# Kernel optimization log

Measured on AMD Instinct MI355X. Metric: run time of the kernel, lower is better.

## Reference

```python
import jax, jax.numpy as jnp
import numpy as np

N = 50000      # nodes
E = 600000     # edges
D_IN = 5
D_H = 128
EPS = 1e-5     # BatchNorm1d default eps


def batch_norm(x, gamma, beta):
    # training-mode BN over the node dimension (biased variance)
    m = jnp.mean(x, axis=0)
    v = jnp.var(x, axis=0)
    return (x - m) * jax.lax.rsqrt(v + EPS) * gamma + beta


def gcn_conv(x, W, b, src, dst, w):
    # PyG GCNConv: linear transform, add self-loops (weight 1),
    # symmetric normalization D^-1/2 A D^-1/2, scatter-add to dst, + bias.
    x = x @ W                                   # [N, out]
    n = x.shape[0]
    loop = jnp.arange(n)
    src = jnp.concatenate([src, loop])
    dst = jnp.concatenate([dst, loop])
    w = jnp.concatenate([w, jnp.ones((n,), w.dtype)])
    deg = jax.ops.segment_sum(w, dst, num_segments=n)
    dis = jnp.where(deg > 0, jax.lax.rsqrt(jnp.maximum(deg, 1e-12)), 0.0)
    norm = dis[src] * w * dis[dst]              # [E+N]
    msgs = norm[:, None] * x[src]               # gather + scale
    return jax.ops.segment_sum(msgs, dst, num_segments=n) + b


def setup_inputs() -> dict:
    key = jax.random.key(0)
    ks = jax.random.split(key, 20)
    s_in = 1.0 / np.sqrt(D_IN)
    s_h = 1.0 / np.sqrt(D_H)
    return {
        "h": jax.random.normal(ks[0], (N, D_IN), jnp.float32),
        "edge_index": jax.random.randint(ks[1], (2, E), 0, N),
        "edge_weight": jax.random.uniform(ks[2], (E,), jnp.float32),
        "g0": 1.0 + 0.1 * jax.random.normal(ks[3], (D_IN,), jnp.float32),
        "be0": 0.1 * jax.random.normal(ks[4], (D_IN,), jnp.float32),
        "W1": jax.random.normal(ks[5], (D_IN, D_H), jnp.float32) * s_in,
        "b1": jax.random.normal(ks[6], (D_H,), jnp.float32) * s_in,
        "g1": 1.0 + 0.1 * jax.random.normal(ks[7], (D_H,), jnp.float32),
        "be1": 0.1 * jax.random.normal(ks[8], (D_H,), jnp.float32),
        "W2": jax.random.normal(ks[9], (D_H, D_H), jnp.float32) * s_h,
        "b2": jax.random.normal(ks[10], (D_H,), jnp.float32) * s_h,
        "g2": 1.0 + 0.1 * jax.random.normal(ks[11], (D_H,), jnp.float32),
        "be2": 0.1 * jax.random.normal(ks[12], (D_H,), jnp.float32),
        "Wmu": jax.random.normal(ks[13], (D_H, D_H), jnp.float32) * s_h,
        "bmu": jax.random.normal(ks[14], (D_H,), jnp.float32) * s_h,
        "Wls": jax.random.normal(ks[15], (D_H, D_H), jnp.float32) * s_h,
        "bls": jax.random.normal(ks[16], (D_H,), jnp.float32) * s_h,
    }


def reference(h, edge_index, edge_weight, g0, be0, W1, b1, g1, be1,
              W2, b2, g2, be2, Wmu, bmu, Wls, bls):
    src, dst = edge_index[0], edge_index[1]
    h = batch_norm(h, g0, be0)
    h = jax.nn.relu(batch_norm(gcn_conv(h, W1, b1, src, dst, edge_weight), g1, be1))
    # dropout p=0.1 treated as eval-mode (identity)
    h = jax.nn.relu(batch_norm(gcn_conv(h, W2, b2, src, dst, edge_weight), g2, be2))
    mu = h @ Wmu + bmu
    log_std = h @ Wls + bls
    return (mu, log_std)
```

## Files before the change

### kernel.cpp

```cpp
#include <hip/hip_runtime.h>

#define N_NODES 50000
#define N_EDGES 600000
#define D_IN 5
#define D_H 128
#define BN_EPS 1e-5f
#define SCAN_BLOCKS ((N_NODES + 255) / 256)
#define DEG_BLOCKS ((N_EDGES + 255) / 256)
#define FIX_SCALE 16777216.0f
#define FIX_INV   (1.0f / 16777216.0f)

typedef __bf16 bf16x8 __attribute__((ext_vector_type(8)));
typedef float  f32x4  __attribute__((ext_vector_type(4)));

__device__ inline unsigned short f2bfb(float f) {
    unsigned u = __builtin_bit_cast(unsigned, f);
    unsigned r = u + 0x7fffu + ((u >> 16) & 1u);
    return (unsigned short)(r >> 16);
}
__device__ inline float bflo(unsigned u) { return __builtin_bit_cast(float, u << 16); }
__device__ inline float bfhi(unsigned u) { return __builtin_bit_cast(float, u & 0xffff0000u); }

__device__ inline void stage_b(const unsigned short* __restrict__ Bt,
                               uint4* __restrict__ lds, int t)
{
#pragma unroll
    for (int i = 0; i < 8; ++i) {
        int slot = i * 256 + t;
        int fid = slot >> 6;
        int l = slot & 63;
        int row = (fid >> 2) * 16 + (l & 15);
        int boff = ((l >> 4) * 16 + (fid & 3) * 64) >> 1;
        lds[slot] = *(const uint4*)(Bt + row * D_H + boff);
    }
}

__global__ __launch_bounds__(256) void k_prep(const float* __restrict__ W2,
                                              const float* __restrict__ Wmu,
                                              const float* __restrict__ Wls,
                                              unsigned short* __restrict__ T2,
                                              unsigned short* __restrict__ Tmu,
                                              unsigned short* __restrict__ Tls,
                                              const float* __restrict__ h,
                                              float* __restrict__ stats0,
                                              const int* __restrict__ dst,
                                              const float* __restrict__ w,
                                              unsigned long long* __restrict__ degcnt,
                                              int* __restrict__ rank)
{
    __shared__ float ss[D_IN], sq[D_IN];
    int b = blockIdx.x;
    int t = threadIdx.x;
    if (b < 192) {
        int mat = b >> 6;
        int idx = (b & 63) * 256 + t;
        const float* W = (mat == 0) ? W2 : (mat == 1) ? Wmu : Wls;
        unsigned short* T = (mat == 0) ? T2 : (mat == 1) ? Tmu : Tls;
        int k = idx >> 7, n = idx & 127;
        T[n * D_H + k] = f2bfb(W[idx]);
    } else if (b < 192 + SCAN_BLOCKS) {
        if (t < D_IN) { ss[t] = 0.f; sq[t] = 0.f; }
        __syncthreads();
        int node = (b - 192) * 256 + t;
        float v[D_IN];
#pragma unroll
        for (int f = 0; f < D_IN; ++f)
            v[f] = (node < N_NODES) ? h[node * D_IN + f] : 0.f;
        int lane = t & 63;
#pragma unroll
        for (int f = 0; f < D_IN; ++f) {
            float s = v[f], q = v[f] * v[f];
            for (int off = 32; off > 0; off >>= 1) {
                s += __shfl_down(s, off);
                q += __shfl_down(q, off);
            }
            if (lane == 0) { atomicAdd(&ss[f], s); atomicAdd(&sq[f], q); }
        }
        __syncthreads();
        if (t < D_IN) {
            atomicAdd(&stats0[t], ss[t]);
            atomicAdd(&stats0[D_IN + t], sq[t]);
        }
    } else {
        int e = (b - 192 - SCAN_BLOCKS) * 256 + t;
        if (e < N_EDGES) {
            int d = dst[e];
            unsigned long long fx = (unsigned long long)(w[e] * FIX_SCALE + 0.5f);
            unsigned long long old = atomicAdd(degcnt + d, (1ull << 40) | fx);
            rank[e] = (int)(old >> 40);
        }
    }
}

__global__ __launch_bounds__(256) void k_scan1(const unsigned long long* __restrict__ degcnt,
                                               float* __restrict__ dis,
                                               int* __restrict__ blocksums)
{
    __shared__ int sm[256];
    int t = threadIdx.x;
    int i = blockIdx.x * 256 + t;
    int c = 0;
    if (i < N_NODES) {
        unsigned long long v = degcnt[i];
        c = (int)(v >> 40);
        float deg = (float)(v & ((1ull << 40) - 1)) * FIX_INV;
        dis[i] = rsqrtf(deg + 1.0f);
    }
    sm[t] = c;
    __syncthreads();
    for (int off = 128; off > 0; off >>= 1) {
        if (t < off) sm[t] += sm[t + off];
        __syncthreads();
    }
    if (t == 0) blocksums[blockIdx.x] = sm[0];
}

__global__ __launch_bounds__(256) void k_scan2(int* __restrict__ blocksums,
                                               int* __restrict__ rowptr)
{
    __shared__ int sm[256];
    int t = threadIdx.x;
    int c = (t < SCAN_BLOCKS) ? blocksums[t] : 0;
    sm[t] = c;
    __syncthreads();
    for (int off = 1; off < 256; off <<= 1) {
        int v = (t >= off) ? sm[t - off] : 0;
        __syncthreads();
        sm[t] += v;
        __syncthreads();
    }
    if (t < SCAN_BLOCKS) blocksums[t] = sm[t] - c;
    if (t == 255) rowptr[N_NODES] = sm[255];
}

__global__ __launch_bounds__(256) void k_scan3(const unsigned long long* __restrict__ degcnt,
                                               int* __restrict__ rowptr,
                                               const int* __restrict__ blocksums)
{
    __shared__ int sm[256];
    int t = threadIdx.x;
    int i = blockIdx.x * 256 + t;
    int c = (i < N_NODES) ? (int)(degcnt[i] >> 40) : 0;
    sm[t] = c;
    __syncthreads();
    for (int off = 1; off < 256; off <<= 1) {
        int v = (t >= off) ? sm[t - off] : 0;
        __syncthreads();
        sm[t] += v;
        __syncthreads();
    }
    if (i < N_NODES)
        rowptr[i] = blocksums[blockIdx.x] + sm[t] - c;
}

__global__ __launch_bounds__(256) void k_fill(const int* __restrict__ src,
                                              const int* __restrict__ dst,
                                              const float* __restrict__ w,
                                              const float* __restrict__ dis,
                                              const int* __restrict__ rowptr,
                                              const int* __restrict__ rank,
                                              int2* __restrict__ csr)
{
    int e = blockIdx.x * blockDim.x + threadIdx.x;
    if (e < N_EDGES) {
        int s = src[e], d = dst[e];
        float pn = dis[s] * w[e];
        int pos = rowptr[d] + rank[e];
        int2 pk;
        pk.x = s;
        pk.y = __builtin_bit_cast(int, pn);
        csr[pos] = pk;
    }
}

__global__ __launch_bounds__(256) void k_agg0(const float* __restrict__ h,
                                              const float* __restrict__ stats,
                                              const float* __restrict__ g0,
                                              const float* __restrict__ be0,
                                              const int* __restrict__ rowptr,
                                              const int2* __restrict__ csr,
                                              const float* __restrict__ dis,
                                              float* __restrict__ agg)
{
    int n = blockIdx.x * blockDim.x + threadIdx.x;
    if (n >= N_NODES) return;
    float sc[D_IN], sh[D_IN];
#pragma unroll
    for (int f = 0; f < D_IN; ++f) {
        float m = stats[f] * (1.0f / N_NODES);
        float var = stats[D_IN + f] * (1.0f / N_NODES) - m * m;
        sc[f] = rsqrtf(var + BN_EPS) * g0[f];
        sh[f] = be0[f] - m * sc[f];
    }
    float dn = dis[n];
    float acc[D_IN];
#pragma unroll
    for (int f = 0; f < D_IN; ++f)
        acc[f] = dn * (h[n * D_IN + f] * sc[f] + sh[f]);
    int e0 = rowptr[n], e1 = rowptr[n + 1];
    for (int e = e0; e < e1; ++e) {
        int2 pk = csr[e];
        int s = pk.x;
        float pn = __builtin_bit_cast(float, pk.y);
#pragma unroll
        for (int f = 0; f < D_IN; ++f)
            acc[f] += pn * (h[s * D_IN + f] * sc[f] + sh[f]);
    }
#pragma unroll
    for (int f = 0; f < D_IN; ++f)
        agg[n * D_IN + f] = dn * acc[f];
}

__global__ __launch_bounds__(256) void k_l1(const float* __restrict__ agg,
                                            const float* __restrict__ W1,
                                            const float* __restrict__ b1,
                                            unsigned short* __restrict__ x,
                                            float* __restrict__ stats)
{
    __shared__ float sm_s[D_H], sm_q[D_H];
    int t = threadIdx.x;
    if (t < D_H) { sm_s[t] = 0.f; sm_q[t] = 0.f; }
    __syncthreads();
    int idx0 = blockIdx.x * 256 + t;
    int f0 = (idx0 & 63) * 2;
    float wa[D_IN], wb[D_IN];
#pragma unroll
    for (int k = 0; k < D_IN; ++k) {
        wa[k] = W1[k * D_H + f0];
        wb[k] = W1[k * D_H + f0 + 1];
    }
    float ba = b1[f0], bb = b1[f0 + 1];
    float s0 = 0.f, q0 = 0.f, s1 = 0.f, q1 = 0.f;
    const int stride = 512 * 256;
    for (int idx = idx0; idx < N_NODES * 64; idx += stride) {
        int n = idx >> 6;
        const float* a = agg + n * D_IN;
        float v0 = ba, v1 = bb;
#pragma unroll
        for (int k = 0; k < D_IN; ++k) { v0 += wa[k] * a[k]; v1 += wb[k] * a[k]; }
        ((unsigned*)x)[idx] = (unsigned)f2bfb(v0) | ((unsigned)f2bfb(v1) << 16);
        s0 += v0; q0 += v0 * v0; s1 += v1; q1 += v1 * v1;
    }
    atomicAdd(&sm_s[f0], s0); atomicAdd(&sm_s[f0 + 1], s1);
    atomicAdd(&sm_q[f0], q0); atomicAdd(&sm_q[f0 + 1], q1);
    __syncthreads();
    if (t < D_H) {
        atomicAdd(stats + t, sm_s[t]);
        atomicAdd(stats + D_H + t, sm_q[t]);
    }
}

__global__ __launch_bounds__(256) void k_agg128(const unsigned short* __restrict__ x,
                                                const float* __restrict__ stats,
                                                const float* __restrict__ g,
                                                const float* __restrict__ be,
                                                const int* __restrict__ rowptr,
                                                const int2* __restrict__ csr,
                                                const float* __restrict__ dis,
                                                unsigned short* __restrict__ outb)
{
    int t = threadIdx.x;
    int n = blockIdx.x * 16 + (t >> 4);
    int f0 = (t & 15) * 8;
    if (n >= N_NODES) return;
    float sc[8], sh[8];
    const float inv = 1.0f / N_NODES;
#pragma unroll
    for (int j = 0; j < 8; ++j) {
        float m = stats[f0 + j] * inv;
        float var = stats[D_H + f0 + j] * inv - m * m;
        sc[j] = rsqrtf(var + BN_EPS) * g[f0 + j];
        sh[j] = be[f0 + j] - m * sc[j];
    }
#define BNR(val, j) fmaxf((val) * sc[j] + sh[j], 0.f)
    float dn = dis[n];
    uint4 hv = *(const uint4*)(x + (size_t)n * D_H + f0);
    float a0 = dn * BNR(bflo(hv.x), 0), a1 = dn * BNR(bfhi(hv.x), 1);
    float a2 = dn * BNR(bflo(hv.y), 2), a3 = dn * BNR(bfhi(hv.y), 3);
    float a4 = dn * BNR(bflo(hv.z), 4), a5 = dn * BNR(bfhi(hv.z), 5);
    float a6 = dn * BNR(bflo(hv.w), 6), a7 = dn * BNR(bfhi(hv.w), 7);
    int e = rowptr[n], e1 = rowptr[n + 1];
    for (; e + 4 <= e1; e += 4) {
        int2 p0 = csr[e + 0], p1 = csr[e + 1], p2 = csr[e + 2], p3 = csr[e + 3];
        float w0 = __builtin_bit_cast(float, p0.y);
        float w1 = __builtin_bit_cast(float, p1.y);
        float w2 = __builtin_bit_cast(float, p2.y);
        float w3 = __builtin_bit_cast(float, p3.y);
        uint4 v0 = *(const uint4*)(x + (size_t)p0.x * D_H + f0);
        uint4 v1 = *(const uint4*)(x + (size_t)p1.x * D_H + f0);
        uint4 v2 = *(const uint4*)(x + (size_t)p2.x * D_H + f0);
        uint4 v3 = *(const uint4*)(x + (size_t)p3.x * D_H + f0);
        a0 += w0 * BNR(bflo(v0.x), 0) + w1 * BNR(bflo(v1.x), 0) + w2 * BNR(bflo(v2.x), 0) + w3 * BNR(bflo(v3.x), 0);
        a1 += w0 * BNR(bfhi(v0.x), 1) + w1 * BNR(bfhi(v1.x), 1) + w2 * BNR(bfhi(v2.x), 1) + w3 * BNR(bfhi(v3.x), 1);
        a2 += w0 * BNR(bflo(v0.y), 2) + w1 * BNR(bflo(v1.y), 2) + w2 * BNR(bflo(v2.y), 2) + w3 * BNR(bflo(v3.y), 2);
        a3 += w0 * BNR(bfhi(v0.y), 3) + w1 * BNR(bfhi(v1.y), 3) + w2 * BNR(bfhi(v2.y), 3) + w3 * BNR(bfhi(v3.y), 3);
        a4 += w0 * BNR(bflo(v0.z), 4) + w1 * BNR(bflo(v1.z), 4) + w2 * BNR(bflo(v2.z), 4) + w3 * BNR(bflo(v3.z), 4);
        a5 += w0 * BNR(bfhi(v0.z), 5) + w1 * BNR(bfhi(v1.z), 5) + w2 * BNR(bfhi(v2.z), 5) + w3 * BNR(bfhi(v3.z), 5);
        a6 += w0 * BNR(bflo(v0.w), 6) + w1 * BNR(bflo(v1.w), 6) + w2 * BNR(bflo(v2.w), 6) + w3 * BNR(bflo(v3.w), 6);
        a7 += w0 * BNR(bfhi(v0.w), 7) + w1 * BNR(bfhi(v1.w), 7) + w2 * BNR(bfhi(v2.w), 7) + w3 * BNR(bfhi(v3.w), 7);
    }
    for (; e < e1; ++e) {
        int2 pk = csr[e];
        float pn = __builtin_bit_cast(float, pk.y);
        uint4 v = *(const uint4*)(x + (size_t)pk.x * D_H + f0);
        a0 += pn * BNR(bflo(v.x), 0); a1 += pn * BNR(bfhi(v.x), 1);
        a2 += pn * BNR(bflo(v.y), 2); a3 += pn * BNR(bfhi(v.y), 3);
        a4 += pn * BNR(bflo(v.z), 4); a5 += pn * BNR(bfhi(v.z), 5);
        a6 += pn * BNR(bflo(v.w), 6); a7 += pn * BNR(bfhi(v.w), 7);
    }
#undef BNR
    uint4 o;
    o.x = (unsigned)f2bfb(dn * a0) | ((unsigned)f2bfb(dn * a1) << 16);
    o.y = (unsigned)f2bfb(dn * a2) | ((unsigned)f2bfb(dn * a3) << 16);
    o.z = (unsigned)f2bfb(dn * a4) | ((unsigned)f2bfb(dn * a5) << 16);
    o.w = (unsigned)f2bfb(dn * a6) | ((unsigned)f2bfb(dn * a7) << 16);
    *(uint4*)(outb + (size_t)n * D_H + f0) = o;
}

__global__ __launch_bounds__(256) void k_gemm_mf(const unsigned short* __restrict__ A,
                                                 const unsigned short* __restrict__ Bt,
                                                 const float* __restrict__ bias,
                                                 unsigned short* __restrict__ C,
                                                 float* __restrict__ stats)
{
    __shared__ uint4 ldsB[2048];
    __shared__ float sm_s[D_H], sm_q[D_H];
    int t = threadIdx.x;
    if (t < D_H) { sm_s[t] = 0.f; sm_q[t] = 0.f; }
    stage_b(Bt, ldsB, t);
    int wave = t >> 6, lane = t & 63;
    int m = lane & 15, quad = lane >> 4;
    int r0 = blockIdx.x * 64 + wave * 16;
    int arow = r0 + m < N_NODES ? r0 + m : N_NODES - 1;
    const bf16x8* ap = (const bf16x8*)(A + (size_t)arow * D_H + quad * 8);
    bf16x8 af[4];
#pragma unroll
    for (int ks = 0; ks < 4; ++ks) af[ks] = ap[ks * 4];
    __syncthreads();
    const bf16x8* bf = (const bf16x8*)ldsB;
    f32x4 acc[8];
#pragma unroll
    for (int ct = 0; ct < 8; ++ct) acc[ct] = (f32x4)(0.f);
#pragma unroll
    for (int ks = 0; ks < 4; ++ks) {
#pragma unroll
        for (int ct = 0; ct < 8; ++ct) {
            acc[ct] = __builtin_amdgcn_mfma_f32_16x16x32_bf16(
                af[ks], bf[(ct * 4 + ks) * 64 + lane], acc[ct], 0, 0, 0);
        }
    }
#pragma unroll
    for (int ct = 0; ct < 8; ++ct) {
        int col = ct * 16 + m;
        float bv = bias[col];
        float s = 0.f, q = 0.f;
#pragma unroll
        for (int r = 0; r < 4; ++r) {
            int rr = r0 + quad * 4 + r;
            if (rr < N_NODES) {
                float v = acc[ct][r] + bv;
                C[(size_t)rr * D_H + col] = f2bfb(v);
                s += v; q += v * v;
            }
        }
        atomicAdd(&sm_s[col], s);
        atomicAdd(&sm_q[col], q);
    }
    __syncthreads();
    if (t < D_H) {
        atomicAdd(stats + t, sm_s[t]);
        atomicAdd(stats + D_H + t, sm_q[t]);
    }
}

__global__ __launch_bounds__(256) void k_gemm_out_mf(const unsigned short* __restrict__ A,
                                                     const float* __restrict__ stats,
                                                     const float* __restrict__ g,
                                                     const float* __restrict__ be,
                                                     const unsigned short* __restrict__ Btmu,
                                                     const float* __restrict__ bmu,
                                                     const unsigned short* __restrict__ Btls,
                                                     const float* __restrict__ bls,
                                                     float* __restrict__ out)
{
    __shared__ uint4 ldsB[2048];
    int t = threadIdx.x;
    int wave = t >> 6, lane = t & 63;
    int m = lane & 15, quad = lane >> 4;
    int r0 = blockIdx.x * 64 + wave * 16;
    int arow = r0 + m < N_NODES ? r0 + m : N_NODES - 1;
    const unsigned short* arowp = A + (size_t)arow * D_H + quad * 8;
    const float inv = 1.0f / N_NODES;
    bf16x8 af[4];
#pragma unroll
    for (int ks = 0; ks < 4; ++ks) {
        uint4 av = *(const uint4*)(arowp + ks * 32);
        float vals[8] = { bflo(av.x), bfhi(av.x), bflo(av.y), bfhi(av.y),
                          bflo(av.z), bfhi(av.z), bflo(av.w), bfhi(av.w) };
        int fb = quad * 8 + ks * 32;
        unsigned short o[8];
#pragma unroll
        for (int j = 0; j < 8; ++j) {
            int f = fb + j;
            float mm = stats[f] * inv;
            float var = stats[D_H + f] * inv - mm * mm;
            float scv = rsqrtf(var + BN_EPS) * g[f];
            float shv = be[f] - mm * scv;
            o[j] = f2bfb(fmaxf(vals[j] * scv + shv, 0.f));
        }
        uint4 pk;
        pk.x = (unsigned)o[0] | ((unsigned)o[1] << 16);
        pk.y = (unsigned)o[2] | ((unsigned)o[3] << 16);
        pk.z = (unsigned)o[4] | ((unsigned)o[5] << 16);
        pk.w = (unsigned)o[6] | ((unsigned)o[7] << 16);
        af[ks] = __builtin_bit_cast(bf16x8, pk);
    }
    const bf16x8* bf = (const bf16x8*)ldsB;
#pragma unroll
    for (int half = 0; half < 2; ++half) {
        if (half) __syncthreads();
        stage_b(half ? Btls : Btmu, ldsB, t);
        __syncthreads();
        const float* bias = half ? bls : bmu;
        float* C = out + (half ? (size_t)N_NODES * D_H : 0);
        f32x4 acc[8];
#pragma unroll
        for (int ct = 0; ct < 8; ++ct) acc[ct] = (f32x4)(0.f);
#pragma unroll
        for (int ks = 0; ks < 4; ++ks) {
#pragma unroll
            for (int ct = 0; ct < 8; ++ct) {
                acc[ct] = __builtin_amdgcn_mfma_f32_16x16x32_bf16(
                    af[ks], bf[(ct * 4 + ks) * 64 + lane], acc[ct], 0, 0, 0);
            }
        }
#pragma unroll
        for (int ct = 0; ct < 8; ++ct) {
            int col = ct * 16 + m;
            float bv = bias[col];
#pragma unroll
            for (int r = 0; r < 4; ++r) {
                int rr = r0 + quad * 4 + r;
                if (rr < N_NODES)
                    C[(size_t)rr * D_H + col] = acc[ct][r] + bv;
            }
        }
    }
}

extern "C" void kernel_launch(void* const* d_in, const int* in_sizes, int n_in,
                              void* d_out, int out_size, void* d_ws, size_t ws_size,
                              hipStream_t stream)
{
    const float* h   = (const float*)d_in[0];
    const int*   eidx = (const int*)d_in[1];
    const float* ew  = (const float*)d_in[2];
    const float* g0  = (const float*)d_in[3];
    const float* be0 = (const float*)d_in[4];
    const float* W1  = (const float*)d_in[5];
    const float* b1  = (const float*)d_in[6];
    const float* g1  = (const float*)d_in[7];
    const float* be1 = (const float*)d_in[8];
    const float* W2  = (const float*)d_in[9];
    const float* b2  = (const float*)d_in[10];
    const float* g2  = (const float*)d_in[11];
    const float* be2 = (const float*)d_in[12];
    const float* Wmu = (const float*)d_in[13];
    const float* bmu = (const float*)d_in[14];
    const float* Wls = (const float*)d_in[15];
    const float* bls = (const float*)d_in[16];
    const int* srcv = eidx;
    const int* dstv = eidx + N_EDGES;
    float* out = (float*)d_out;

    char* ws = (char*)d_ws;
    size_t off = 0;
    auto alloc = [&](size_t bytes) -> char* {
        char* p = ws + off;
        off += (bytes + 255) & ~(size_t)255;
        return p;
    };
    float* stats0  = (float*)alloc(16 * 4);
    float* stats1  = (float*)alloc(256 * 4);
    float* stats2  = (float*)alloc(256 * 4);
    unsigned long long* degcnt = (unsigned long long*)alloc(N_NODES * 8);
    size_t zero_bytes = off;
    int*   rowptr  = (int*)  alloc((N_NODES + 1) * 4);
    float* dis     = (float*)alloc(N_NODES * 4);
    int*   rank    = (int*)  alloc((size_t)N_EDGES * 4);
    int*   blocksums = (int*)alloc(256 * 4);
    int2*  csr     = (int2*) alloc((size_t)N_EDGES * 8);
    float* agg0    = (float*)alloc(N_NODES * D_IN * 4);
    unsigned short* x1h  = (unsigned short*)alloc((size_t)N_NODES * D_H * 2);
    unsigned short* aggh = (unsigned short*)alloc((size_t)N_NODES * D_H * 2);
    unsigned short* c2h  = (unsigned short*)alloc((size_t)N_NODES * D_H * 2);
    unsigned short* Wt2   = (unsigned short*)alloc(D_H * D_H * 2);
    unsigned short* Wtmu  = (unsigned short*)alloc(D_H * D_H * 2);
    unsigned short* Wtls  = (unsigned short*)alloc(D_H * D_H * 2);
    (void)ws_size; (void)in_sizes; (void)n_in; (void)out_size;

    hipMemsetAsync(d_ws, 0, zero_bytes, stream);

    k_prep<<<192 + SCAN_BLOCKS + DEG_BLOCKS, 256, 0, stream>>>(
        W2, Wmu, Wls, Wt2, Wtmu, Wtls, h, stats0, dstv, ew, degcnt, rank);
    k_scan1<<<SCAN_BLOCKS, 256, 0, stream>>>(degcnt, dis, blocksums);
    k_scan2<<<1, 256, 0, stream>>>(blocksums, rowptr);
    k_scan3<<<SCAN_BLOCKS, 256, 0, stream>>>(degcnt, rowptr, blocksums);
    k_fill<<<DEG_BLOCKS, 256, 0, stream>>>(srcv, dstv, ew, dis, rowptr, rank, csr);
    k_agg0<<<SCAN_BLOCKS, 256, 0, stream>>>(h, stats0, g0, be0, rowptr, csr, dis, agg0);
    k_l1<<<512, 256, 0, stream>>>(agg0, W1, b1, x1h, stats1);
    k_agg128<<<(N_NODES + 15) / 16, 256, 0, stream>>>(x1h, stats1, g1, be1,
                                                      rowptr, csr, dis, aggh);
    k_gemm_mf<<<(N_NODES + 63) / 64, 256, 0, stream>>>(aggh, Wt2, b2, c2h, stats2);
    k_gemm_out_mf<<<(N_NODES + 63) / 64, 256, 0, stream>>>(c2h, stats2, g2, be2,
                                                           Wtmu, bmu, Wtls, bls, out);
}
```

Baseline: 282.4 us.

## Derive layer-1 BN stats from aggregated-input moments and merge scan kernels

Layer-1 batch-norm statistics are now computed analytically from the first and second moments (sum and Gram matrix) of the 5-wide aggregated input, reduced in k_agg0. This lets k_l1 apply BN and ReLU before storing bf16, so k_agg128 no longer applies BN per gathered neighbour. The single-block scan2 kernel is folded into scan3, with each block summing its predecessor block totals. The moment-based variance (E[x^2]-m^2 through W1) may lose precision in fp32, and rowptr[N] is hard-coded to N_EDGES.

```diff
diff --git a/kernel.cpp b/kernel.cpp
--- a/kernel.cpp
+++ b/kernel.cpp
@@ -115,31 +115,24 @@
     if (t == 0) blocksums[blockIdx.x] = sm[0];
 }
 
-__global__ __launch_bounds__(256) void k_scan2(int* __restrict__ blocksums,
-                                               int* __restrict__ rowptr)
-{
-    __shared__ int sm[256];
-    int t = threadIdx.x;
-    int c = (t < SCAN_BLOCKS) ? blocksums[t] : 0;
-    sm[t] = c;
-    __syncthreads();
-    for (int off = 1; off < 256; off <<= 1) {
-        int v = (t >= off) ? sm[t - off] : 0;
-        __syncthreads();
-        sm[t] += v;
-        __syncthreads();
-    }
-    if (t < SCAN_BLOCKS) blocksums[t] = sm[t] - c;
-    if (t == 255) rowptr[N_NODES] = sm[255];
-}
-
 __global__ __launch_bounds__(256) void k_scan3(const unsigned long long* __restrict__ degcnt,
                                                int* __restrict__ rowptr,
                                                const int* __restrict__ blocksums)
 {
     __shared__ int sm[256];
-    int t = threadIdx.x;
-    int i = blockIdx.x * 256 + t;
+    __shared__ int soff;
+    int t = threadIdx.x;
+    int bid = blockIdx.x;
+    int pre = (t < bid) ? blocksums[t] : 0;
+    sm[t] = pre;
+    __syncthreads();
+    for (int off = 128; off > 0; off >>= 1) {
+        if (t < off) sm[t] += sm[t + off];
+        __syncthreads();
+    }
+    if (t == 0) soff = sm[0];
+    __syncthreads();
+    int i = bid * 256 + t;
     int c = (i < N_NODES) ? (int)(degcnt[i] >> 40) : 0;
     sm[t] = c;
     __syncthreads();
@@ -150,7 +143,9 @@
         __syncthreads();
     }
     if (i < N_NODES)
-        rowptr[i] = blocksums[blockIdx.x] + sm[t] - c;
+        rowptr[i] = soff + sm[t] - c;
+    if (bid == 0 && t == 0)
+        rowptr[N_NODES] = N_EDGES;
 }
 
 __global__ __launch_bounds__(256) void k_fill(const int* __restrict__ src,
@@ -180,47 +175,80 @@
                                               const int* __restrict__ rowptr,
                                               const int2* __restrict__ csr,
                                               const float* __restrict__ dis,
-                                              float* __restrict__ agg)
-{
-    int n = blockIdx.x * blockDim.x + threadIdx.x;
-    if (n >= N_NODES) return;
-    float sc[D_IN], sh[D_IN];
-#pragma unroll
-    for (int f = 0; f < D_IN; ++f) {
-        float m = stats[f] * (1.0f / N_NODES);
-        float var = stats[D_IN + f] * (1.0f / N_NODES) - m * m;
-        sc[f] = rsqrtf(var + BN_EPS) * g0[f];
-        sh[f] = be0[f] - m * sc[f];
-    }
-    float dn = dis[n];
-    float acc[D_IN];
-#pragma unroll
-    for (int f = 0; f < D_IN; ++f)
-        acc[f] = dn * (h[n * D_IN + f] * sc[f] + sh[f]);
-    int e0 = rowptr[n], e1 = rowptr[n + 1];
-    for (int e = e0; e < e1; ++e) {
-        int2 pk = csr[e];
-        int s = pk.x;
-        float pn = __builtin_bit_cast(float, pk.y);
+                                              float* __restrict__ agg,
+                                              float* __restrict__ statsA)
+{
+    __shared__ float sA[20];
+    int t = threadIdx.x;
+    if (t < 20) sA[t] = 0.f;
+    __syncthreads();
+    int n = blockIdx.x * 256 + t;
+    float av[D_IN] = {0.f, 0.f, 0.f, 0.f, 0.f};
+    if (n < N_NODES) {
+        float sc[D_IN], sh[D_IN];
+#pragma unroll
+        for (int f = 0; f < D_IN; ++f) {
+            float m = stats[f] * (1.0f / N_NODES);
+            float var = stats[D_IN + f] * (1.0f / N_NODES) - m * m;
+            sc[f] = rsqrtf(var + BN_EPS) * g0[f];
+            sh[f] = be0[f] - m * sc[f];
+        }
+        float dn = dis[n];
+        float acc[D_IN];
 #pragma unroll
         for (int f = 0; f < D_IN; ++f)
-            acc[f] += pn * (h[s * D_IN + f] * sc[f] + sh[f]);
-    }
-#pragma unroll
-    for (int f = 0; f < D_IN; ++f)
-        agg[n * D_IN + f] = dn * acc[f];
+            acc[f] = dn * (h[n * D_IN + f] * sc[f] + sh[f]);
+        int e0 = rowptr[n], e1 = rowptr[n + 1];
+        for (int e = e0; e < e1; ++e) {
+            int2 pk = csr[e];
+            int s = pk.x;
+            float pn = __builtin_bit_cast(float, pk.y);
+#pragma unroll
+            for (int f = 0; f < D_IN; ++f)
+                acc[f] += pn * (h[s * D_IN + f] * sc[f] + sh[f]);
+        }
+#pragma unroll
+        for (int f = 0; f < D_IN; ++f) {
+            float o = dn * acc[f];
+            agg[n * D_IN + f] = o;
+            av[f] = o;
+        }
+    }
+    float red[20];
+#pragma unroll
+    for (int f = 0; f < D_IN; ++f) red[f] = av[f];
+    {
+        int idx = D_IN;
+#pragma unroll
+        for (int k = 0; k < D_IN; ++k)
+#pragma unroll
+            for (int l = k; l < D_IN; ++l)
+                red[idx++] = av[k] * av[l];
+    }
+#pragma unroll
+    for (int off = 32; off > 0; off >>= 1) {
+#pragma unroll
+        for (int i = 0; i < 20; ++i)
+            red[i] += __shfl_down(red[i], off);
+    }
+    if ((t & 63) == 0) {
+#pragma unroll
+        for (int i = 0; i < 20; ++i)
+            atomicAdd(&sA[i], red[i]);
+    }
+    __syncthreads();
+    if (t < 20) atomicAdd(statsA + t, sA[t]);
 }
 
 __global__ __launch_bounds__(256) void k_l1(const float* __restrict__ agg,
                                             const float* __restrict__ W1,
                                             const float* __restrict__ b1,
-                                            unsigned short* __restrict__ x,
-                                            float* __restrict__ stats)
-{
-    __shared__ float sm_s[D_H], sm_q[D_H];
-    int t = threadIdx.x;
-    if (t < D_H) { sm_s[t] = 0.f; sm_q[t] = 0.f; }
-    __syncthreads();
+                                            const float* __restrict__ g1,
+                                            const float* __restrict__ be1,
+                                            const float* __restrict__ statsA,
+                                            unsigned short* __restrict__ x)
+{
+    int t = threadIdx.x;
     int idx0 = blockIdx.x * 256 + t;
     int f0 = (idx0 & 63) * 2;
     float wa[D_IN], wb[D_IN];
@@ -230,7 +258,43 @@
         wb[k] = W1[k * D_H + f0 + 1];
     }
     float ba = b1[f0], bb = b1[f0 + 1];
-    float s0 = 0.f, q0 = 0.f, s1 = 0.f, q1 = 0.f;
+
+    const float inv = 1.0f / N_NODES;
+    float S1[D_IN];
+#pragma unroll
+    for (int k = 0; k < D_IN; ++k) S1[k] = statsA[k];
+    float M[D_IN][D_IN];
+    {
+        int idx = D_IN;
+#pragma unroll
+        for (int k = 0; k < D_IN; ++k)
+#pragma unroll
+            for (int l = k; l < D_IN; ++l) {
+                float v = statsA[idx++];
+                M[k][l] = v;
+                M[l][k] = v;
+            }
+    }
+    float t1a = 0.f, t1b = 0.f, qa = 0.f, qb = 0.f;
+#pragma unroll
+    for (int k = 0; k < D_IN; ++k) { t1a += wa[k] * S1[k]; t1b += wb[k] * S1[k]; }
+#pragma unroll
+    for (int k = 0; k < D_IN; ++k) {
+        float ra = 0.f, rb = 0.f;
+#pragma unroll
+        for (int l = 0; l < D_IN; ++l) { ra += M[k][l] * wa[l]; rb += M[k][l] * wb[l]; }
+        qa += wa[k] * ra;
+        qb += wb[k] * rb;
+    }
+    float ma = t1a * inv, mb = t1b * inv;
+    float mua = ma + ba, mub = mb + bb;
+    float vara = fmaxf(qa * inv - ma * ma, 0.f);
+    float varb = fmaxf(qb * inv - mb * mb, 0.f);
+    float sca = rsqrtf(vara + BN_EPS) * g1[f0];
+    float scb = rsqrtf(varb + BN_EPS) * g1[f0 + 1];
+    float sha = be1[f0] - mua * sca;
+    float shb = be1[f0 + 1] - mub * scb;
+
     const int stride = 512 * 256;
     for (int idx = idx0; idx < N_NODES * 64; idx += stride) {
         int n = idx >> 6;
@@ -238,22 +302,13 @@
         float v0 = ba, v1 = bb;
 #pragma unroll
         for (int k = 0; k < D_IN; ++k) { v0 += wa[k] * a[k]; v1 += wb[k] * a[k]; }
+        v0 = fmaxf(v0 * sca + sha, 0.f);
+        v1 = fmaxf(v1 * scb + shb, 0.f);
         ((unsigned*)x)[idx] = (unsigned)f2bfb(v0) | ((unsigned)f2bfb(v1) << 16);
-        s0 += v0; q0 += v0 * v0; s1 += v1; q1 += v1 * v1;
-    }
-    atomicAdd(&sm_s[f0], s0); atomicAdd(&sm_s[f0 + 1], s1);
-    atomicAdd(&sm_q[f0], q0); atomicAdd(&sm_q[f0 + 1], q1);
-    __syncthreads();
-    if (t < D_H) {
-        atomicAdd(stats + t, sm_s[t]);
-        atomicAdd(stats + D_H + t, sm_q[t]);
     }
 }
 
 __global__ __launch_bounds__(256) void k_agg128(const unsigned short* __restrict__ x,
-                                                const float* __restrict__ stats,
-                                                const float* __restrict__ g,
-                                                const float* __restrict__ be,
                                                 const int* __restrict__ rowptr,
                                                 const int2* __restrict__ csr,
                                                 const float* __restrict__ dis,
@@ -263,22 +318,12 @@
     int n = blockIdx.x * 16 + (t >> 4);
     int f0 = (t & 15) * 8;
     if (n >= N_NODES) return;
-    float sc[8], sh[8];
-    const float inv = 1.0f / N_NODES;
-#pragma unroll
-    for (int j = 0; j < 8; ++j) {
-        float m = stats[f0 + j] * inv;
-        float var = stats[D_H + f0 + j] * inv - m * m;
-        sc[j] = rsqrtf(var + BN_EPS) * g[f0 + j];
-        sh[j] = be[f0 + j] - m * sc[j];
-    }
-#define BNR(val, j) fmaxf((val) * sc[j] + sh[j], 0.f)
     float dn = dis[n];
     uint4 hv = *(const uint4*)(x + (size_t)n * D_H + f0);
-    float a0 = dn * BNR(bflo(hv.x), 0), a1 = dn * BNR(bfhi(hv.x), 1);
-    float a2 = dn * BNR(bflo(hv.y), 2), a3 = dn * BNR(bfhi(hv.y), 3);
-    float a4 = dn * BNR(bflo(hv.z), 4), a5 = dn * BNR(bfhi(hv.z), 5);
-    float a6 = dn * BNR(bflo(hv.w), 6), a7 = dn * BNR(bfhi(hv.w), 7);
+    float a0 = dn * bflo(hv.x), a1 = dn * bfhi(hv.x);
+    float a2 = dn * bflo(hv.y), a3 = dn * bfhi(hv.y);
+    float a4 = dn * bflo(hv.z), a5 = dn * bfhi(hv.z);
+    float a6 = dn * bflo(hv.w), a7 = dn * bfhi(hv.w);
     int e = rowptr[n], e1 = rowptr[n + 1];
     for (; e + 4 <= e1; e += 4) {
         int2 p0 = csr[e + 0], p1 = csr[e + 1], p2 = csr[e + 2], p3 = csr[e + 3];
@@ -290,25 +335,24 @@
         uint4 v1 = *(const uint4*)(x + (size_t)p1.x * D_H + f0);
         uint4 v2 = *(const uint4*)(x + (size_t)p2.x * D_H + f0);
         uint4 v3 = *(const uint4*)(x + (size_t)p3.x * D_H + f0);
-        a0 += w0 * BNR(bflo(v0.x), 0) + w1 * BNR(bflo(v1.x), 0) + w2 * BNR(bflo(v2.x), 0) + w3 * BNR(bflo(v3.x), 0);
-        a1 += w0 * BNR(bfhi(v0.x), 1) + w1 * BNR(bfhi(v1.x), 1) + w2 * BNR(bfhi(v2.x), 1) + w3 * BNR(bfhi(v3.x), 1);
-        a2 += w0 * BNR(bflo(v0.y), 2) + w1 * BNR(bflo(v1.y), 2) + w2 * BNR(bflo(v2.y), 2) + w3 * BNR(bflo(v3.y), 2);
-        a3 += w0 * BNR(bfhi(v0.y), 3) + w1 * BNR(bfhi(v1.y), 3) + w2 * BNR(bfhi(v2.y), 3) + w3 * BNR(bfhi(v3.y), 3);
-        a4 += w0 * BNR(bflo(v0.z), 4) + w1 * BNR(bflo(v1.z), 4) + w2 * BNR(bflo(v2.z), 4) + w3 * BNR(bflo(v3.z), 4);
-        a5 += w0 * BNR(bfhi(v0.z), 5) + w1 * BNR(bfhi(v1.z), 5) + w2 * BNR(bfhi(v2.z), 5) + w3 * BNR(bfhi(v3.z), 5);
-        a6 += w0 * BNR(bflo(v0.w), 6) + w1 * BNR(bflo(v1.w), 6) + w2 * BNR(bflo(v2.w), 6) + w3 * BNR(bflo(v3.w), 6);
-        a7 += w0 * BNR(bfhi(v0.w), 7) + w1 * BNR(bfhi(v1.w), 7) + w2 * BNR(bfhi(v2.w), 7) + w3 * BNR(bfhi(v3.w), 7);
+        a0 += w0 * bflo(v0.x) + w1 * bflo(v1.x) + w2 * bflo(v2.x) + w3 * bflo(v3.x);
+        a1 += w0 * bfhi(v0.x) + w1 * bfhi(v1.x) + w2 * bfhi(v2.x) + w3 * bfhi(v3.x);
+        a2 += w0 * bflo(v0.y) + w1 * bflo(v1.y) + w2 * bflo(v2.y) + w3 * bflo(v3.y);
+        a3 += w0 * bfhi(v0.y) + w1 * bfhi(v1.y) + w2 * bfhi(v2.y) + w3 * bfhi(v3.y);
+        a4 += w0 * bflo(v0.z) + w1 * bflo(v1.z) + w2 * bflo(v2.z) + w3 * bflo(v3.z);
+        a5 += w0 * bfhi(v0.z) + w1 * bfhi(v1.z) + w2 * bfhi(v2.z) + w3 * bfhi(v3.z);
+        a6 += w0 * bflo(v0.w) + w1 * bflo(v1.w) + w2 * bflo(v2.w) + w3 * bflo(v3.w);
+        a7 += w0 * bfhi(v0.w) + w1 * bfhi(v1.w) + w2 * bfhi(v2.w) + w3 * bfhi(v3.w);
     }
     for (; e < e1; ++e) {
         int2 pk = csr[e];
         float pn = __builtin_bit_cast(float, pk.y);
         uint4 v = *(const uint4*)(x + (size_t)pk.x * D_H + f0);
-        a0 += pn * BNR(bflo(v.x), 0); a1 += pn * BNR(bfhi(v.x), 1);
-        a2 += pn * BNR(bflo(v.y), 2); a3 += pn * BNR(bfhi(v.y), 3);
-        a4 += pn * BNR(bflo(v.z), 4); a5 += pn * BNR(bfhi(v.z), 5);
-        a6 += pn * BNR(bflo(v.w), 6); a7 += pn * BNR(bfhi(v.w), 7);
-    }
-#undef BNR
+        a0 += pn * bflo(v.x); a1 += pn * bfhi(v.x);
+        a2 += pn * bflo(v.y); a3 += pn * bfhi(v.y);
+        a4 += pn * bflo(v.z); a5 += pn * bfhi(v.z);
+        a6 += pn * bflo(v.w); a7 += pn * bfhi(v.w);
+    }
     uint4 o;
     o.x = (unsigned)f2bfb(dn * a0) | ((unsigned)f2bfb(dn * a1) << 16);
     o.y = (unsigned)f2bfb(dn * a2) | ((unsigned)f2bfb(dn * a3) << 16);
@@ -481,7 +525,7 @@
         return p;
     };
     float* stats0  = (float*)alloc(16 * 4);
-    float* stats1  = (float*)alloc(256 * 4);
+    float* statsA  = (float*)alloc(32 * 4);
     float* stats2  = (float*)alloc(256 * 4);
     unsigned long long* degcnt = (unsigned long long*)alloc(N_NODES * 8);
     size_t zero_bytes = off;
@@ -504,13 +548,12 @@
     k_prep<<<192 + SCAN_BLOCKS + DEG_BLOCKS, 256, 0, stream>>>(
         W2, Wmu, Wls, Wt2, Wtmu, Wtls, h, stats0, dstv, ew, degcnt, rank);
     k_scan1<<<SCAN_BLOCKS, 256, 0, stream>>>(degcnt, dis, blocksums);
-    k_scan2<<<1, 256, 0, stream>>>(blocksums, rowptr);
     k_scan3<<<SCAN_BLOCKS, 256, 0, stream>>>(degcnt, rowptr, blocksums);
     k_fill<<<DEG_BLOCKS, 256, 0, stream>>>(srcv, dstv, ew, dis, rowptr, rank, csr);
-    k_agg0<<<SCAN_BLOCKS, 256, 0, stream>>>(h, stats0, g0, be0, rowptr, csr, dis, agg0);
-    k_l1<<<512, 256, 0, stream>>>(agg0, W1, b1, x1h, stats1);
-    k_agg128<<<(N_NODES + 15) / 16, 256, 0, stream>>>(x1h, stats1, g1, be1,
-                                                      rowptr, csr, dis, aggh);
+    k_agg0<<<SCAN_BLOCKS, 256, 0, stream>>>(h, stats0, g0, be0, rowptr, csr, dis,
+                                            agg0, statsA);
+    k_l1<<<512, 256, 0, stream>>>(agg0, W1, b1, g1, be1, statsA, x1h);
+    k_agg128<<<(N_NODES + 15) / 16, 256, 0, stream>>>(x1h, rowptr, csr, dis, aggh);
     k_gemm_mf<<<(N_NODES + 63) / 64, 256, 0, stream>>>(aggh, Wt2, b2, c2h, stats2);
     k_gemm_out_mf<<<(N_NODES + 63) / 64, 256, 0, stream>>>(c2h, stats2, g2, be2,
                                                            Wtmu, bmu, Wtls, bls, out);
```

After: 262.7 us (median of 2 runs). -7.0%, faster.
